# Kernel optimization log

Hardware: AMD Instinct MI355X
Metric: run time of the kernel (lower is better)

Reference implementation:

```python
import jax, jax.numpy as jnp
import numpy as np

N = 100000       # num nodes
E = 3200000      # train message edges (avg degree 32)
EP = 1600000     # pos (and neg) decode edges
F_IN = 128       # node feature dim
H1, H2 = 50, 10  # GCN layer widths from source


def setup_inputs() -> dict:
    key = jax.random.key(0)
    ks = jax.random.split(key, 6)
    x = jax.random.normal(ks[0], (N, F_IN), dtype=jnp.float32)
    train_pos_edge_index = jax.random.randint(ks[1], (2, E), 0, N)
    pos_edge_index = jax.random.randint(ks[2], (2, EP), 0, N)
    neg_edge_index = jax.random.randint(ks[3], (2, EP), 0, N)
    W1 = jax.random.normal(ks[4], (F_IN, H1), dtype=jnp.float32) / np.float32(np.sqrt(F_IN))
    b1 = jnp.zeros((H1,), jnp.float32)
    W2 = jax.random.normal(ks[5], (H1, H2), dtype=jnp.float32) / np.float32(np.sqrt(H1))
    b2 = jnp.zeros((H2,), jnp.float32)
    return {"x": x, "W1": W1, "b1": b1, "W2": W2, "b2": b2,
            "train_pos_edge_index": train_pos_edge_index,
            "pos_edge_index": pos_edge_index,
            "neg_edge_index": neg_edge_index}


def gcn_conv(x, W, b, src, dst, num_nodes):
    # x: [N, Fin] -> transform first (PyG GCNConv), then normalize+aggregate.
    h = x @ W                                                        # [N, Fout]
    deg = jax.ops.segment_sum(jnp.ones(src.shape, h.dtype), dst,
                              num_segments=num_nodes)                # in-degree incl self-loops
    dinv = jnp.where(deg > 0, jax.lax.rsqrt(deg), 0.0)
    norm = dinv[src] * dinv[dst]                                     # [E']
    msgs = h[src] * norm[:, None]                                    # gather + scale
    out = jax.ops.segment_sum(msgs, dst, num_segments=num_nodes)     # scatter-add
    return out + b


def reference(x, W1, b1, W2, b2, train_pos_edge_index, pos_edge_index, neg_edge_index):
    # GCNConv adds self-loops to the message edge set.
    loops = jnp.arange(N, dtype=train_pos_edge_index.dtype)
    src = jnp.concatenate([train_pos_edge_index[0], loops])
    dst = jnp.concatenate([train_pos_edge_index[1], loops])
    # encode(): conv1 -> relu -> conv2
    h = jax.nn.relu(gcn_conv(x, W1, b1, src, dst, N))                # [N, 50]
    z = gcn_conv(h, W2, b2, src, dst, N)                             # [N, 10]
    # decode(): concat pos/neg edges, edge-wise dot product of endpoint embeddings
    ei = jnp.concatenate([pos_edge_index, neg_edge_index], axis=-1)  # [2, 2*EP]
    logits = jnp.sum(z[ei[0]] * z[ei[1]], axis=-1)                   # [2*EP]
    return logits
```

## Files before the change

### kernel.cpp

```cpp
#include <hip/hip_runtime.h>

#define FIN 128
#define H1_ 50
#define H2_ 10
#define ST2S 16

#define BKT_SHIFT 7
#define BKT_W 128
#define NB_MAX 800
#define SB_SHIFT 11
#define SB_W 2048
#define NSB_MAX 64
#define SB_CAP 81920
#define P1_CHUNK 8192
#define P1F_CHUNK 4096


__device__ inline float bf2f(unsigned int u16) {
    union { unsigned int i; float f; } c; c.i = u16 << 16; return c.f;
}
__device__ inline unsigned short f2bf(float f) {
    union { float f; unsigned int i; } c; c.f = f;
    unsigned int x = c.i;
    return (unsigned short)((x + 0x7FFFu + ((x >> 16) & 1u)) >> 16);
}
__device__ inline void unpack8(uint4 v, float* f) {
    f[0] = bf2f(v.x & 0xFFFFu); f[1] = bf2f(v.x >> 16);
    f[2] = bf2f(v.y & 0xFFFFu); f[3] = bf2f(v.y >> 16);
    f[4] = bf2f(v.z & 0xFFFFu); f[5] = bf2f(v.z >> 16);
    f[6] = bf2f(v.w & 0xFFFFu); f[7] = bf2f(v.w >> 16);
}


__global__ __launch_bounds__(256) void partition_sb(const int* __restrict__ src,
                                                    const int* __restrict__ dst,
                                                    int* __restrict__ sbcnt,
                                                    int* __restrict__ bcnt,
                                                    int* __restrict__ pairbuf1,
                                                    int E, int nsb) {
    __shared__ int lh[NB_MAX];
    __shared__ int lhs[NSB_MAX];
    __shared__ int lbs[NSB_MAX];
    int tid = threadIdx.x;
    for (int i = tid; i < NB_MAX; i += 256) lh[i] = 0;
    if (tid < NSB_MAX) lhs[tid] = 0;
    __syncthreads();
    int lo = blockIdx.x * P1_CHUNK;
    int hi = min(lo + P1_CHUNK, E);
    for (int e = lo + tid; e < hi; e += 256)
        atomicAdd(&lh[dst[e] >> BKT_SHIFT], 1);
    __syncthreads();
    if (tid < nsb) {
        int c = 0;
#pragma unroll
        for (int j = 0; j < 16; ++j) {
            int idx = tid * 16 + j;
            c += (idx < NB_MAX) ? lh[idx] : 0;
        }
        lbs[tid] = c ? (tid * SB_CAP + atomicAdd(&sbcnt[tid], c)) : 0;
    }
    for (int i = tid; i < NB_MAX; i += 256) {
        int c = lh[i];
        if (c) atomicAdd(&bcnt[i], c);
    }
    __syncthreads();
    for (int e = lo + tid; e < hi; e += 256) {
        int sv = src[e], d = dst[e];
        int b = d >> SB_SHIFT;
        int r = atomicAdd(&lhs[b], 1);
        pairbuf1[lbs[b] + r] = sv | ((d & (SB_W - 1)) << 17);
    }
}

__global__ __launch_bounds__(256) void bucket_scan(const int* __restrict__ bcnt,
                                                   int* __restrict__ bbase,
                                                   int* __restrict__ bcursor,
                                                   int nb2, int E) {
    __shared__ int s[256];
    int t = threadIdx.x;
    int base = t * 4;
    int v0 = (base + 0 < nb2) ? bcnt[base + 0] : 0;
    int v1 = (base + 1 < nb2) ? bcnt[base + 1] : 0;
    int v2 = (base + 2 < nb2) ? bcnt[base + 2] : 0;
    int v3 = (base + 3 < nb2) ? bcnt[base + 3] : 0;
    int tsum = v0 + v1 + v2 + v3;
    s[t] = tsum;
    __syncthreads();
    for (int off = 1; off < 256; off <<= 1) {
        int x = (t >= off) ? s[t - off] : 0;
        __syncthreads();
        s[t] += x;
        __syncthreads();
    }
    int excl = s[t] - tsum;
    if (t == 0) bbase[nb2] = E;
    if (base + 0 < nb2) { bbase[base + 0] = excl; bcursor[base + 0] = excl; }
    excl += v0;
    if (base + 1 < nb2) { bbase[base + 1] = excl; bcursor[base + 1] = excl; }
    excl += v1;
    if (base + 2 < nb2) { bbase[base + 2] = excl; bcursor[base + 2] = excl; }
    excl += v2;
    if (base + 3 < nb2) { bbase[base + 3] = excl; bcursor[base + 3] = excl; }
}


__global__ __launch_bounds__(256) void partition_fine(const int* __restrict__ pairbuf1,
                                                      const int* __restrict__ sbcnt,
                                                      int* __restrict__ bcursor,
                                                      int* __restrict__ pairbuf2) {
    int sb = blockIdx.y;
    int cnt = sbcnt[sb];
    int rel = blockIdx.x * P1F_CHUNK;
    if (rel >= cnt) return;
    int lo = sb * SB_CAP + rel;
    int hi = sb * SB_CAP + min(rel + P1F_CHUNK, cnt);
    __shared__ int lh[16];
    __shared__ int lb[16];
    int tid = threadIdx.x;
    if (tid < 16) lh[tid] = 0;
    __syncthreads();
    for (int j = lo + tid; j < hi; j += 256)
        atomicAdd(&lh[(pairbuf1[j] >> 17) >> BKT_SHIFT], 1);
    __syncthreads();
    if (tid < 16) {
        int c = lh[tid];
        lb[tid] = c ? atomicAdd(&bcursor[sb * 16 + tid], c) : 0;
        lh[tid] = 0;
    }
    __syncthreads();
    for (int j = lo + tid; j < hi; j += 256) {
        int p = pairbuf1[j];
        int din = p >> 17;
        int fb = din >> BKT_SHIFT;
        int r = atomicAdd(&lh[fb], 1);
        pairbuf2[lb[fb] + r] = (p & 0x1FFFF) | ((din & (BKT_W - 1)) << 17);
    }
}


__global__ __launch_bounds__(256) void bucket_fill_scan(const int* __restrict__ pairbuf,
                                                        const int* __restrict__ bbase,
                                                        int* __restrict__ rowptr,
                                                        float* __restrict__ dinv,
                                                        int* __restrict__ ecol,
                                                        int N, int E) {
    __shared__ int cnt[BKT_W];
    __shared__ int sc[BKT_W];
    __shared__ int cur[BKT_W];
    int b = blockIdx.x;
    int base_node = b << BKT_SHIFT;
    int nnodes = min(BKT_W, N - base_node);
    int tid = threadIdx.x;
    if (tid < BKT_W) cnt[tid] = 0;
    __syncthreads();
    int lo = bbase[b], hi = bbase[b + 1];
    for (int j = lo + tid; j < hi; j += 256)
        atomicAdd(&cnt[pairbuf[j] >> 17], 1);
    __syncthreads();
    int c = (tid < BKT_W) ? cnt[tid] : 0;
    if (tid < BKT_W) sc[tid] = c;
    __syncthreads();
    for (int off = 1; off < BKT_W; off <<= 1) {
        int xv = (tid >= off && tid < BKT_W) ? sc[tid - off] : 0;
        __syncthreads();
        if (tid < BKT_W) sc[tid] += xv;
        __syncthreads();
    }
    if (tid < nnodes) {
        int rp = lo + sc[tid] - c;
        rowptr[base_node + tid] = rp;
        cur[tid] = rp;
        dinv[base_node + tid] = rsqrtf(1.0f + (float)c);
    }
    __syncthreads();
    for (int j = lo + tid; j < hi; j += 256) {
        int p = pairbuf[j];
        int pos = atomicAdd(&cur[p >> 17], 1);
        ecol[pos] = p & 0x1FFFF;
    }
    if (b == (int)gridDim.x - 1 && tid == 0) rowptr[N] = E;
}


#define G1_NODES 128
#define SX_PITCH 132
#define KCHUNK 32
__global__ __launch_bounds__(256) void gemm1_kernel(const float* __restrict__ x,
                                                    const float* __restrict__ W1,
                                                    const float* __restrict__ dinv,
                                                    unsigned short* __restrict__ st1p, int N) {
    __shared__ float sX[G1_NODES * SX_PITCH];
    __shared__ float sW[KCHUNK * 64];
    int tid = threadIdx.x;
    int nb = blockIdx.x * G1_NODES;
    {
        const float4* x4 = (const float4*)(x + (size_t)nb * FIN);
        for (int i = tid; i < G1_NODES * 32; i += 256) {
            int ln = i >> 5, kk = i & 31;
            float4 v = (nb + ln < N) ? x4[(size_t)ln * 32 + kk]
                                     : make_float4(0.f, 0.f, 0.f, 0.f);
            *(float4*)(&sX[ln * SX_PITCH + kk * 4]) = v;
        }
    }
    int q = tid >> 3;
    int g = tid & 7;
    const float* xr0 = &sX[(4 * q + 0) * SX_PITCH];
    const float* xr1 = &sX[(4 * q + 1) * SX_PITCH];
    const float* xr2 = &sX[(4 * q + 2) * SX_PITCH];
    const float* xr3 = &sX[(4 * q + 3) * SX_PITCH];
    float acc[4][8];
#pragma unroll
    for (int i = 0; i < 4; ++i)
#pragma unroll
        for (int j = 0; j < 8; ++j) acc[i][j] = 0.0f;

    for (int kc = 0; kc < FIN / KCHUNK; ++kc) {
        __syncthreads();
        for (int i = tid; i < KCHUNK * 64; i += 256) {
            int k = i >> 6, f = i & 63;
            sW[i] = (f < H1_) ? W1[(kc * KCHUNK + k) * H1_ + f] : 0.0f;
        }
        __syncthreads();
        int kb = kc * KCHUNK;
#pragma unroll 4
        for (int k = 0; k < KCHUNK; ++k) {
            float xv0 = xr0[kb + k];
            float xv1 = xr1[kb + k];
            float xv2 = xr2[kb + k];
            float xv3 = xr3[kb + k];
            const float* w = &sW[k * 64 + g * 8];
#pragma unroll
            for (int j = 0; j < 8; ++j) {
                float wv = w[j];
                acc[0][j] = fmaf(xv0, wv, acc[0][j]);
                acc[1][j] = fmaf(xv1, wv, acc[1][j]);
                acc[2][j] = fmaf(xv2, wv, acc[2][j]);
                acc[3][j] = fmaf(xv3, wv, acc[3][j]);
            }
        }
    }
#pragma unroll
    for (int i = 0; i < 4; ++i) {
        int node = nb + 4 * q + i;
        if (node >= N) continue;
        float di = dinv[node];
        unsigned short o[8];
#pragma unroll
        for (int j = 0; j < 8; ++j) o[j] = f2bf(acc[i][j] * di);
        uint4 pk;
        pk.x = (unsigned)o[0] | ((unsigned)o[1] << 16);
        pk.y = (unsigned)o[2] | ((unsigned)o[3] << 16);
        pk.z = (unsigned)o[4] | ((unsigned)o[5] << 16);
        pk.w = (unsigned)o[6] | ((unsigned)o[7] << 16);
        *(uint4*)(st1p + (size_t)node * 64 + g * 8) = pk;
    }
}


__global__ __launch_bounds__(256) void csr_aggregate1(const unsigned short* __restrict__ st,
                                                      const int* __restrict__ rowptr,
                                                      const int* __restrict__ ecol,
                                                      const float* __restrict__ dinv,
                                                      const float* __restrict__ b,
                                                      float* __restrict__ out, int N) {
    int idx = blockIdx.x * blockDim.x + threadIdx.x;
    if (idx >= N * 8) return;
    int d = idx >> 3;
    int g = idx & 7;
    if (g == 7) return;
    const unsigned short* row = st + g * 8;
    float acc[8];
    {
        uint4 sv = *(const uint4*)(row + (size_t)d * 64);
        float f[8]; unpack8(sv, f);
#pragma unroll
        for (int k = 0; k < 8; ++k) acc[k] = f[k];
    }
    int j = rowptr[d], end = rowptr[d + 1];
    for (; j + 3 < end; j += 4) {
        int s0 = ecol[j], s1 = ecol[j + 1], s2 = ecol[j + 2], s3 = ecol[j + 3];
        uint4 v0 = *(const uint4*)(row + (size_t)s0 * 64);
        uint4 v1 = *(const uint4*)(row + (size_t)s1 * 64);
        uint4 v2 = *(const uint4*)(row + (size_t)s2 * 64);
        uint4 v3 = *(const uint4*)(row + (size_t)s3 * 64);
        float f0[8], f1[8], f2[8], f3[8];
        unpack8(v0, f0); unpack8(v1, f1); unpack8(v2, f2); unpack8(v3, f3);
#pragma unroll
        for (int k = 0; k < 8; ++k) acc[k] += (f0[k] + f1[k]) + (f2[k] + f3[k]);
    }
    for (; j < end; ++j) {
        uint4 v = *(const uint4*)(row + (size_t)ecol[j] * 64);
        float f[8]; unpack8(v, f);
#pragma unroll
        for (int k = 0; k < 8; ++k) acc[k] += f[k];
    }
    float vd = dinv[d];
    int fb = 8 * g;
    float* op = out + (size_t)d * H1_ + fb;
    int npair = (g == 6) ? 1 : 4;
#pragma unroll
    for (int k = 0; k < 4; ++k) {
        if (k >= npair) break;
        float r0 = fmaxf(fmaf(vd, acc[2 * k],     b[fb + 2 * k]),     0.0f);
        float r1 = fmaxf(fmaf(vd, acc[2 * k + 1], b[fb + 2 * k + 1]), 0.0f);
        *(float2*)(op + 2 * k) = make_float2(r0, r1);
    }
}


__global__ __launch_bounds__(256) void gemm2_kernel(const float* __restrict__ h,
                                                    const float* __restrict__ W2,
                                                    const float* __restrict__ dinv,
                                                    float* __restrict__ st2, int n16) {
    __shared__ float sW[H1_ * H2_];
    int tid = threadIdx.x;
    for (int i = tid; i < H1_ * H2_; i += 256) sW[i] = W2[i];
    __syncthreads();
    int idx = blockIdx.x * blockDim.x + tid;
    if (idx >= n16) return;
    int node = idx >> 4;
    int f    = idx & 15;
    if (f >= H2_) { st2[idx] = 0.0f; return; }
    const float* hr = &h[(size_t)node * H1_];
    float acc = 0.0f;
#pragma unroll
    for (int k = 0; k < H1_; ++k) acc = fmaf(hr[k], sW[k * H2_ + f], acc);
    st2[idx] = acc * dinv[node];
}


__global__ __launch_bounds__(256) void csr_aggregate2(const float* __restrict__ st,
                                                      const int* __restrict__ rowptr,
                                                      const int* __restrict__ ecol,
                                                      const float* __restrict__ dinv,
                                                      const float* __restrict__ b,
                                                      float* __restrict__ z0,
                                                      float* __restrict__ z1, int N) {
    int idx = blockIdx.x * blockDim.x + threadIdx.x;
    if (idx >= N * 4) return;
    int d = idx >> 2;
    int g = idx & 3;
    if (g == 3) return;
    const float* row = st + g * 4;
    float4 acc = *(const float4*)(row + (size_t)d * ST2S);
    int j = rowptr[d], end = rowptr[d + 1];
    for (; j + 3 < end; j += 4) {
        int s0 = ecol[j], s1 = ecol[j + 1], s2 = ecol[j + 2], s3 = ecol[j + 3];
        float4 a0 = *(const float4*)(row + (size_t)s0 * ST2S);
        float4 a1 = *(const float4*)(row + (size_t)s1 * ST2S);
        float4 a2 = *(const float4*)(row + (size_t)s2 * ST2S);
        float4 a3 = *(const float4*)(row + (size_t)s3 * ST2S);
        acc.x += (a0.x + a1.x) + (a2.x + a3.x);
        acc.y += (a0.y + a1.y) + (a2.y + a3.y);
        acc.z += (a0.z + a1.z) + (a2.z + a3.z);
        acc.w += (a0.w + a1.w) + (a2.w + a3.w);
    }
    for (; j < end; ++j) {
        float4 a = *(const float4*)(row + (size_t)ecol[j] * ST2S);
        acc.x += a.x; acc.y += a.y; acc.z += a.z; acc.w += a.w;
    }
    float vd = dinv[d];
    if (g < 2) {
        float4 r;
        r.x = fmaf(vd, acc.x, b[4 * g + 0]);
        r.y = fmaf(vd, acc.y, b[4 * g + 1]);
        r.z = fmaf(vd, acc.z, b[4 * g + 2]);
        r.w = fmaf(vd, acc.w, b[4 * g + 3]);
        *(float4*)(z0 + (size_t)d * 8 + 4 * g) = r;
    } else {
        float2 r;
        r.x = fmaf(vd, acc.x, b[8]);
        r.y = fmaf(vd, acc.y, b[9]);
        *(float2*)(z1 + (size_t)d * 2) = r;
    }
}


__global__ __launch_bounds__(256) void decode_kernel(const float* __restrict__ z0,
                                                     const float* __restrict__ z1,
                                                     const int* __restrict__ pos,
                                                     const int* __restrict__ neg,
                                                     float* __restrict__ logits, int EP) {
    int i = blockIdx.x * blockDim.x + threadIdx.x;
    if (i >= 2 * EP) return;
    int a, b;
    if (i < EP) {
        a = __builtin_nontemporal_load(&pos[i]);
        b = __builtin_nontemporal_load(&pos[EP + i]);
    } else {
        int j = i - EP;
        a = __builtin_nontemporal_load(&neg[j]);
        b = __builtin_nontemporal_load(&neg[EP + j]);
    }
    const float4* za = (const float4*)(z0 + (size_t)a * 8);
    const float4* zb = (const float4*)(z0 + (size_t)b * 8);
    float4 a0 = za[0];
    float4 a1 = za[1];
    float4 b0 = zb[0];
    float4 b1 = zb[1];
    float2 a2 = *(const float2*)(z1 + (size_t)a * 2);
    float2 b2 = *(const float2*)(z1 + (size_t)b * 2);
    float acc = a0.x * b0.x;
    acc = fmaf(a0.y, b0.y, acc);
    acc = fmaf(a0.z, b0.z, acc);
    acc = fmaf(a0.w, b0.w, acc);
    acc = fmaf(a1.x, b1.x, acc);
    acc = fmaf(a1.y, b1.y, acc);
    acc = fmaf(a1.z, b1.z, acc);
    acc = fmaf(a1.w, b1.w, acc);
    acc = fmaf(a2.x, b2.x, acc);
    acc = fmaf(a2.y, b2.y, acc);
    __builtin_nontemporal_store(acc, &logits[i]);
}


extern "C" void kernel_launch(void* const* d_in, const int* in_sizes, int n_in,
                              void* d_out, int out_size, void* d_ws, size_t ws_size,
                              hipStream_t stream) {
    const float* x   = (const float*)d_in[0];
    const float* W1  = (const float*)d_in[1];
    const float* b1  = (const float*)d_in[2];
    const float* W2  = (const float*)d_in[3];
    const float* b2  = (const float*)d_in[4];
    const int* train = (const int*)d_in[5];
    const int* pos   = (const int*)d_in[6];
    const int* neg   = (const int*)d_in[7];

    const int N  = in_sizes[0] / FIN;
    const int E  = in_sizes[5] / 2;
    const int EP = in_sizes[6] / 2;

    const int* tsrc = train;
    const int* tdst = train + E;

    size_t off = 0;
    int* rowptr   = (int*)d_ws;              off += (size_t)N + 1;
    int* bcnt     = (int*)d_ws + off;        off += NB_MAX;
    int* sbcnt    = (int*)d_ws + off;        off += NSB_MAX;
    int* bbase    = (int*)d_ws + off;        off += NB_MAX + 1;
    int* bcursor  = (int*)d_ws + off;        off += NB_MAX;
    float* dinv   = (float*)d_ws + off;      off += N;
    off = (off + 15) & ~(size_t)15;
    float* regA   = (float*)d_ws + off;      off += (size_t)32 * N;
    float* regB   = (float*)d_ws + off;
    int* pairbuf2 = (int*)regA;
    unsigned short* st1p = (unsigned short*)regA;
    float* st2    = regA;
    float* z0     = regA + (size_t)16 * N;
    float* z1     = regA + (size_t)24 * N;
    int* pairbuf1 = (int*)regB;
    float* out1   = regB;
    int* ecol     = (int*)d_out;
    float* logits = (float*)d_out;

    const int NB2 = (N + BKT_W - 1) >> BKT_SHIFT;
    const int NSB = (N + SB_W - 1) >> SB_SHIFT;
    const int P1B = (E + P1_CHUNK - 1) / P1_CHUNK;
    const int P1FB = (SB_CAP + P1F_CHUNK - 1) / P1F_CHUNK;

    hipMemsetAsync(bcnt, 0, (NB_MAX + NSB_MAX) * sizeof(int), stream);
    partition_sb<<<P1B, 256, 0, stream>>>(tsrc, tdst, sbcnt, bcnt, pairbuf1, E, NSB);
    bucket_scan<<<1, 256, 0, stream>>>(bcnt, bbase, bcursor, NB2, E);
    partition_fine<<<dim3(P1FB, NSB), 256, 0, stream>>>(pairbuf1, sbcnt, bcursor, pairbuf2);
    bucket_fill_scan<<<NB2, 256, 0, stream>>>(pairbuf2, bbase, rowptr, dinv, ecol, N, E);

    gemm1_kernel<<<(N + G1_NODES - 1) / G1_NODES, 256, 0, stream>>>(x, W1, dinv, st1p, N);
    csr_aggregate1<<<(N * 8 + 255) / 256, 256, 0, stream>>>(
        st1p, rowptr, ecol, dinv, b1, out1, N);

    gemm2_kernel<<<(N * 16 + 255) / 256, 256, 0, stream>>>(out1, W2, dinv, st2, N * 16);
    csr_aggregate2<<<(N * 4 + 255) / 256, 256, 0, stream>>>(
        st2, rowptr, ecol, dinv, b2, z0, z1, N);

    decode_kernel<<<(2 * EP + 255) / 256, 256, 0, stream>>>(z0, z1, pos, neg, logits, EP);
}
```

Measured before the change: 478.3 us.

## Split aggregation tables into feature slices so each gather set fits in cache

The layer-1 bf16 message table is stored as three 16-feature slices of 32 bytes per node plus a 2-feature tail. The layer-1 aggregation runs as four launches, one per slice, and layer-2 is split the same way into an 8-wide and a 2-wide table. Each launch gathers from a much smaller table (about 3.2 MB instead of 12.8 MB), so the random neighbour reads are more likely to hit in L2/MALL. In exchange the CSR index array is re-read once per slice, and edge-index loads and output stores are marked nontemporal.

```diff
diff --git a/kernel.cpp b/kernel.cpp
--- a/kernel.cpp
+++ b/kernel.cpp
@@ -3,7 +3,6 @@
 #define FIN 128
 #define H1_ 50
 #define H2_ 10
-#define ST2S 16
 
 #define BKT_SHIFT 7
 #define BKT_W 128
@@ -15,6 +14,9 @@
 #define P1_CHUNK 8192
 #define P1F_CHUNK 4096
 
+typedef float f32x2 __attribute__((ext_vector_type(2)));
+typedef float f32x4 __attribute__((ext_vector_type(4)));
+
 
 __device__ inline float bf2f(unsigned int u16) {
     union { unsigned int i; float f; } c; c.i = u16 << 16; return c.f;
@@ -29,6 +31,14 @@
     f[2] = bf2f(v.y & 0xFFFFu); f[3] = bf2f(v.y >> 16);
     f[4] = bf2f(v.z & 0xFFFFu); f[5] = bf2f(v.z >> 16);
     f[6] = bf2f(v.w & 0xFFFFu); f[7] = bf2f(v.w >> 16);
+}
+__device__ inline void nt_store2(float* p, float a, float b) {
+    f32x2 v; v.x = a; v.y = b;
+    __builtin_nontemporal_store(v, (f32x2*)p);
+}
+__device__ inline void nt_store4(float* p, float a, float b, float c, float d) {
+    f32x4 v; v.x = a; v.y = b; v.z = c; v.w = d;
+    __builtin_nontemporal_store(v, (f32x4*)p);
 }
 
 
@@ -188,7 +198,7 @@
 __global__ __launch_bounds__(256) void gemm1_kernel(const float* __restrict__ x,
                                                     const float* __restrict__ W1,
                                                     const float* __restrict__ dinv,
-                                                    unsigned short* __restrict__ st1p, int N) {
+                                                    unsigned short* __restrict__ st1, int N) {
     __shared__ float sX[G1_NODES * SX_PITCH];
     __shared__ float sW[KCHUNK * 64];
     int tid = threadIdx.x;
@@ -243,75 +253,119 @@
     for (int i = 0; i < 4; ++i) {
         int node = nb + 4 * q + i;
         if (node >= N) continue;
+        if (g == 7) continue;
         float di = dinv[node];
         unsigned short o[8];
 #pragma unroll
         for (int j = 0; j < 8; ++j) o[j] = f2bf(acc[i][j] * di);
-        uint4 pk;
-        pk.x = (unsigned)o[0] | ((unsigned)o[1] << 16);
-        pk.y = (unsigned)o[2] | ((unsigned)o[3] << 16);
-        pk.z = (unsigned)o[4] | ((unsigned)o[5] << 16);
-        pk.w = (unsigned)o[6] | ((unsigned)o[7] << 16);
-        *(uint4*)(st1p + (size_t)node * 64 + g * 8) = pk;
-    }
-}
-
-
-__global__ __launch_bounds__(256) void csr_aggregate1(const unsigned short* __restrict__ st,
+        if (g < 6) {
+            uint4 pk;
+            pk.x = (unsigned)o[0] | ((unsigned)o[1] << 16);
+            pk.y = (unsigned)o[2] | ((unsigned)o[3] << 16);
+            pk.z = (unsigned)o[4] | ((unsigned)o[5] << 16);
+            pk.w = (unsigned)o[6] | ((unsigned)o[7] << 16);
+            *(uint4*)(st1 + (size_t)(g >> 1) * 16 * N + (size_t)node * 16 + (g & 1) * 8) = pk;
+        } else {
+            unsigned int pk = (unsigned)o[0] | ((unsigned)o[1] << 16);
+            *(unsigned int*)(st1 + (size_t)48 * N + (size_t)node * 2) = pk;
+        }
+    }
+}
+
+
+__global__ __launch_bounds__(256) void csr_agg1_slice(const unsigned short* __restrict__ tab,
                                                       const int* __restrict__ rowptr,
                                                       const int* __restrict__ ecol,
                                                       const float* __restrict__ dinv,
                                                       const float* __restrict__ b,
-                                                      float* __restrict__ out, int N) {
+                                                      float* __restrict__ out,
+                                                      int N) {
     int idx = blockIdx.x * blockDim.x + threadIdx.x;
-    if (idx >= N * 8) return;
-    int d = idx >> 3;
-    int g = idx & 7;
-    if (g == 7) return;
-    const unsigned short* row = st + g * 8;
+    if (idx >= N * 2) return;
+    int d = idx >> 1;
+    int g = idx & 1;
+    const unsigned short* row = tab + g * 8;
     float acc[8];
     {
-        uint4 sv = *(const uint4*)(row + (size_t)d * 64);
+        uint4 sv = *(const uint4*)(row + (size_t)d * 16);
         float f[8]; unpack8(sv, f);
 #pragma unroll
         for (int k = 0; k < 8; ++k) acc[k] = f[k];
     }
     int j = rowptr[d], end = rowptr[d + 1];
     for (; j + 3 < end; j += 4) {
-        int s0 = ecol[j], s1 = ecol[j + 1], s2 = ecol[j + 2], s3 = ecol[j + 3];
-        uint4 v0 = *(const uint4*)(row + (size_t)s0 * 64);
-        uint4 v1 = *(const uint4*)(row + (size_t)s1 * 64);
-        uint4 v2 = *(const uint4*)(row + (size_t)s2 * 64);
-        uint4 v3 = *(const uint4*)(row + (size_t)s3 * 64);
+        int s0 = __builtin_nontemporal_load(&ecol[j]);
+        int s1 = __builtin_nontemporal_load(&ecol[j + 1]);
+        int s2 = __builtin_nontemporal_load(&ecol[j + 2]);
+        int s3 = __builtin_nontemporal_load(&ecol[j + 3]);
+        uint4 v0 = *(const uint4*)(row + (size_t)s0 * 16);
+        uint4 v1 = *(const uint4*)(row + (size_t)s1 * 16);
+        uint4 v2 = *(const uint4*)(row + (size_t)s2 * 16);
+        uint4 v3 = *(const uint4*)(row + (size_t)s3 * 16);
         float f0[8], f1[8], f2[8], f3[8];
         unpack8(v0, f0); unpack8(v1, f1); unpack8(v2, f2); unpack8(v3, f3);
 #pragma unroll
         for (int k = 0; k < 8; ++k) acc[k] += (f0[k] + f1[k]) + (f2[k] + f3[k]);
     }
     for (; j < end; ++j) {
-        uint4 v = *(const uint4*)(row + (size_t)ecol[j] * 64);
+        int s = __builtin_nontemporal_load(&ecol[j]);
+        uint4 v = *(const uint4*)(row + (size_t)s * 16);
         float f[8]; unpack8(v, f);
 #pragma unroll
         for (int k = 0; k < 8; ++k) acc[k] += f[k];
     }
     float vd = dinv[d];
-    int fb = 8 * g;
-    float* op = out + (size_t)d * H1_ + fb;
-    int npair = (g == 6) ? 1 : 4;
+    float* op = out + (size_t)d * H1_ + 8 * g;
 #pragma unroll
     for (int k = 0; k < 4; ++k) {
-        if (k >= npair) break;
-        float r0 = fmaxf(fmaf(vd, acc[2 * k],     b[fb + 2 * k]),     0.0f);
-        float r1 = fmaxf(fmaf(vd, acc[2 * k + 1], b[fb + 2 * k + 1]), 0.0f);
-        *(float2*)(op + 2 * k) = make_float2(r0, r1);
-    }
+        float r0 = fmaxf(fmaf(vd, acc[2 * k],     b[8 * g + 2 * k]),     0.0f);
+        float r1 = fmaxf(fmaf(vd, acc[2 * k + 1], b[8 * g + 2 * k + 1]), 0.0f);
+        nt_store2(op + 2 * k, r0, r1);
+    }
+}
+
+
+__global__ __launch_bounds__(256) void csr_agg1_mini(const unsigned short* __restrict__ tab,
+                                                     const int* __restrict__ rowptr,
+                                                     const int* __restrict__ ecol,
+                                                     const float* __restrict__ dinv,
+                                                     const float* __restrict__ b,
+                                                     float* __restrict__ out, int N) {
+    int d = blockIdx.x * blockDim.x + threadIdx.x;
+    if (d >= N) return;
+    unsigned int sv = *(const unsigned int*)(tab + (size_t)d * 2);
+    float acc0 = bf2f(sv & 0xFFFFu), acc1 = bf2f(sv >> 16);
+    int j = rowptr[d], end = rowptr[d + 1];
+    for (; j + 3 < end; j += 4) {
+        int s0 = __builtin_nontemporal_load(&ecol[j]);
+        int s1 = __builtin_nontemporal_load(&ecol[j + 1]);
+        int s2 = __builtin_nontemporal_load(&ecol[j + 2]);
+        int s3 = __builtin_nontemporal_load(&ecol[j + 3]);
+        unsigned int v0 = *(const unsigned int*)(tab + (size_t)s0 * 2);
+        unsigned int v1 = *(const unsigned int*)(tab + (size_t)s1 * 2);
+        unsigned int v2 = *(const unsigned int*)(tab + (size_t)s2 * 2);
+        unsigned int v3 = *(const unsigned int*)(tab + (size_t)s3 * 2);
+        acc0 += (bf2f(v0 & 0xFFFFu) + bf2f(v1 & 0xFFFFu)) + (bf2f(v2 & 0xFFFFu) + bf2f(v3 & 0xFFFFu));
+        acc1 += (bf2f(v0 >> 16) + bf2f(v1 >> 16)) + (bf2f(v2 >> 16) + bf2f(v3 >> 16));
+    }
+    for (; j < end; ++j) {
+        int s = __builtin_nontemporal_load(&ecol[j]);
+        unsigned int v = *(const unsigned int*)(tab + (size_t)s * 2);
+        acc0 += bf2f(v & 0xFFFFu);
+        acc1 += bf2f(v >> 16);
+    }
+    float vd = dinv[d];
+    float r0 = fmaxf(fmaf(vd, acc0, b[48]), 0.0f);
+    float r1 = fmaxf(fmaf(vd, acc1, b[49]), 0.0f);
+    nt_store2(out + (size_t)d * H1_ + 48, r0, r1);
 }
 
 
 __global__ __launch_bounds__(256) void gemm2_kernel(const float* __restrict__ h,
                                                     const float* __restrict__ W2,
                                                     const float* __restrict__ dinv,
-                                                    float* __restrict__ st2, int n16) {
+                                                    float* __restrict__ st2a,
+                                                    float* __restrict__ st2b, int n16) {
     __shared__ float sW[H1_ * H2_];
     int tid = threadIdx.x;
     for (int i = tid; i < H1_ * H2_; i += 256) sW[i] = W2[i];
@@ -320,59 +374,87 @@
     if (idx >= n16) return;
     int node = idx >> 4;
     int f    = idx & 15;
-    if (f >= H2_) { st2[idx] = 0.0f; return; }
+    if (f >= H2_) return;
     const float* hr = &h[(size_t)node * H1_];
     float acc = 0.0f;
 #pragma unroll
     for (int k = 0; k < H1_; ++k) acc = fmaf(hr[k], sW[k * H2_ + f], acc);
-    st2[idx] = acc * dinv[node];
-}
-
-
-__global__ __launch_bounds__(256) void csr_aggregate2(const float* __restrict__ st,
-                                                      const int* __restrict__ rowptr,
-                                                      const int* __restrict__ ecol,
-                                                      const float* __restrict__ dinv,
-                                                      const float* __restrict__ b,
-                                                      float* __restrict__ z0,
-                                                      float* __restrict__ z1, int N) {
+    float v = acc * dinv[node];
+    if (f < 8) st2a[(size_t)node * 8 + f] = v;
+    else       st2b[(size_t)node * 2 + (f - 8)] = v;
+}
+
+
+__global__ __launch_bounds__(256) void csr_agg2_a(const float* __restrict__ st,
+                                                  const int* __restrict__ rowptr,
+                                                  const int* __restrict__ ecol,
+                                                  const float* __restrict__ dinv,
+                                                  const float* __restrict__ b,
+                                                  float* __restrict__ z0, int N) {
     int idx = blockIdx.x * blockDim.x + threadIdx.x;
-    if (idx >= N * 4) return;
-    int d = idx >> 2;
-    int g = idx & 3;
-    if (g == 3) return;
+    if (idx >= N * 2) return;
+    int d = idx >> 1;
+    int g = idx & 1;
     const float* row = st + g * 4;
-    float4 acc = *(const float4*)(row + (size_t)d * ST2S);
+    float4 acc = *(const float4*)(row + (size_t)d * 8);
     int j = rowptr[d], end = rowptr[d + 1];
     for (; j + 3 < end; j += 4) {
-        int s0 = ecol[j], s1 = ecol[j + 1], s2 = ecol[j + 2], s3 = ecol[j + 3];
-        float4 a0 = *(const float4*)(row + (size_t)s0 * ST2S);
-        float4 a1 = *(const float4*)(row + (size_t)s1 * ST2S);
-        float4 a2 = *(const float4*)(row + (size_t)s2 * ST2S);
-        float4 a3 = *(const float4*)(row + (size_t)s3 * ST2S);
+        int s0 = __builtin_nontemporal_load(&ecol[j]);
+        int s1 = __builtin_nontemporal_load(&ecol[j + 1]);
+        int s2 = __builtin_nontemporal_load(&ecol[j + 2]);
+        int s3 = __builtin_nontemporal_load(&ecol[j + 3]);
+        float4 a0 = *(const float4*)(row + (size_t)s0 * 8);
+        float4 a1 = *(const float4*)(row + (size_t)s1 * 8);
+        float4 a2 = *(const float4*)(row + (size_t)s2 * 8);
+        float4 a3 = *(const float4*)(row + (size_t)s3 * 8);
         acc.x += (a0.x + a1.x) + (a2.x + a3.x);
         acc.y += (a0.y + a1.y) + (a2.y + a3.y);
         acc.z += (a0.z + a1.z) + (a2.z + a3.z);
         acc.w += (a0.w + a1.w) + (a2.w + a3.w);
     }
     for (; j < end; ++j) {
-        float4 a = *(const float4*)(row + (size_t)ecol[j] * ST2S);
+        int s = __builtin_nontemporal_load(&ecol[j]);
+        float4 a = *(const float4*)(row + (size_t)s * 8);
         acc.x += a.x; acc.y += a.y; acc.z += a.z; acc.w += a.w;
     }
     float vd = dinv[d];
-    if (g < 2) {
-        float4 r;
-        r.x = fmaf(vd, acc.x, b[4 * g + 0]);
-        r.y = fmaf(vd, acc.y, b[4 * g + 1]);
-        r.z = fmaf(vd, acc.z, b[4 * g + 2]);
-        r.w = fmaf(vd, acc.w, b[4 * g + 3]);
-        *(float4*)(z0 + (size_t)d * 8 + 4 * g) = r;
-    } else {
-        float2 r;
-        r.x = fmaf(vd, acc.x, b[8]);
-        r.y = fmaf(vd, acc.y, b[9]);
-        *(float2*)(z1 + (size_t)d * 2) = r;
-    }
+    nt_store4(z0 + (size_t)d * 8 + 4 * g,
+              fmaf(vd, acc.x, b[4 * g + 0]),
+              fmaf(vd, acc.y, b[4 * g + 1]),
+              fmaf(vd, acc.z, b[4 * g + 2]),
+              fmaf(vd, acc.w, b[4 * g + 3]));
+}
+
+
+__global__ __launch_bounds__(256) void csr_agg2_b(const float* __restrict__ st,
+                                                  const int* __restrict__ rowptr,
+                                                  const int* __restrict__ ecol,
+                                                  const float* __restrict__ dinv,
+                                                  const float* __restrict__ b,
+                                                  float* __restrict__ z1, int N) {
+    int d = blockIdx.x * blockDim.x + threadIdx.x;
+    if (d >= N) return;
+    float2 acc = *(const float2*)(st + (size_t)d * 2);
+    int j = rowptr[d], end = rowptr[d + 1];
+    for (; j + 3 < end; j += 4) {
+        int s0 = __builtin_nontemporal_load(&ecol[j]);
+        int s1 = __builtin_nontemporal_load(&ecol[j + 1]);
+        int s2 = __builtin_nontemporal_load(&ecol[j + 2]);
+        int s3 = __builtin_nontemporal_load(&ecol[j + 3]);
+        float2 a0 = *(const float2*)(st + (size_t)s0 * 2);
+        float2 a1 = *(const float2*)(st + (size_t)s1 * 2);
+        float2 a2 = *(const float2*)(st + (size_t)s2 * 2);
+        float2 a3 = *(const float2*)(st + (size_t)s3 * 2);
+        acc.x += (a0.x + a1.x) + (a2.x + a3.x);
+        acc.y += (a0.y + a1.y) + (a2.y + a3.y);
+    }
+    for (; j < end; ++j) {
+        int s = __builtin_nontemporal_load(&ecol[j]);
+        float2 a = *(const float2*)(st + (size_t)s * 2);
+        acc.x += a.x; acc.y += a.y;
+    }
+    float vd = dinv[d];
+    nt_store2(z1 + (size_t)d * 2, fmaf(vd, acc.x, b[8]), fmaf(vd, acc.y, b[9]));
 }
 
 
@@ -444,10 +526,11 @@
     float* regA   = (float*)d_ws + off;      off += (size_t)32 * N;
     float* regB   = (float*)d_ws + off;
     int* pairbuf2 = (int*)regA;
-    unsigned short* st1p = (unsigned short*)regA;
-    float* st2    = regA;
-    float* z0     = regA + (size_t)16 * N;
-    float* z1     = regA + (size_t)24 * N;
+    unsigned short* st1 = (unsigned short*)regA;
+    float* st2a   = regA;
+    float* st2b   = regA + (size_t)8 * N;
+    float* z0     = regA + (size_t)10 * N;
+    float* z1     = regA + (size_t)18 * N;
     int* pairbuf1 = (int*)regB;
     float* out1   = regB;
     int* ecol     = (int*)d_out;
@@ -464,13 +547,16 @@
     partition_fine<<<dim3(P1FB, NSB), 256, 0, stream>>>(pairbuf1, sbcnt, bcursor, pairbuf2);
     bucket_fill_scan<<<NB2, 256, 0, stream>>>(pairbuf2, bbase, rowptr, dinv, ecol, N, E);
 
-    gemm1_kernel<<<(N + G1_NODES - 1) / G1_NODES, 256, 0, stream>>>(x, W1, dinv, st1p, N);
-    csr_aggregate1<<<(N * 8 + 255) / 256, 256, 0, stream>>>(
-        st1p, rowptr, ecol, dinv, b1, out1, N);
-
-    gemm2_kernel<<<(N * 16 + 255) / 256, 256, 0, stream>>>(out1, W2, dinv, st2, N * 16);
-    csr_aggregate2<<<(N * 4 + 255) / 256, 256, 0, stream>>>(
-        st2, rowptr, ecol, dinv, b2, z0, z1, N);
+    gemm1_kernel<<<(N + G1_NODES - 1) / G1_NODES, 256, 0, stream>>>(x, W1, dinv, st1, N);
+    for (int s = 0; s < 3; ++s)
+        csr_agg1_slice<<<(N * 2 + 255) / 256, 256, 0, stream>>>(
+            st1 + (size_t)s * 16 * N, rowptr, ecol, dinv, b1 + 16 * s, out1 + 16 * s, N);
+    csr_agg1_mini<<<(N + 255) / 256, 256, 0, stream>>>(
+        st1 + (size_t)48 * N, rowptr, ecol, dinv, b1, out1, N);
+
+    gemm2_kernel<<<(N * 16 + 255) / 256, 256, 0, stream>>>(out1, W2, dinv, st2a, st2b, N * 16);
+    csr_agg2_a<<<(N * 2 + 255) / 256, 256, 0, stream>>>(st2a, rowptr, ecol, dinv, b2, z0, N);
+    csr_agg2_b<<<(N + 255) / 256, 256, 0, stream>>>(st2b, rowptr, ecol, dinv, b2, z1, N);
 
     decode_kernel<<<(2 * EP + 255) / 256, 256, 0, stream>>>(z0, z1, pos, neg, logits, EP);
 }
```

New measurement: 615.8 us. +28.7%, slower.

## Sort CSR columns by source chunk and narrow aggregate1 to 2 features per thread

Applied to the files above, without the earlier changes.

The bucket fill now counts each destination's edges in 16 sub-bins keyed by source-index range. It prefix-sums those bins so ecol comes out roughly sorted by source within each row, which should improve gather locality in later aggregations. csr_aggregate1 changes from 8 bf16 features per thread with 16-byte loads to 2 features per thread with 4-byte loads, across 25 threads per node. This gives more parallelism and adjacent threads read contiguous bytes of the same source row, at the cost of more threads re-reading the edge list. gemm1 also skips storing the unused padding group.

```diff
diff --git a/kernel.cpp b/kernel.cpp
--- a/kernel.cpp
+++ b/kernel.cpp
@@ -14,6 +14,7 @@
 #define SB_CAP 81920
 #define P1_CHUNK 8192
 #define P1F_CHUNK 4096
+#define SCH 16
 
 
 __device__ inline float bf2f(unsigned int u16) {
@@ -23,12 +24,6 @@
     union { float f; unsigned int i; } c; c.f = f;
     unsigned int x = c.i;
     return (unsigned short)((x + 0x7FFFu + ((x >> 16) & 1u)) >> 16);
-}
-__device__ inline void unpack8(uint4 v, float* f) {
-    f[0] = bf2f(v.x & 0xFFFFu); f[1] = bf2f(v.x >> 16);
-    f[2] = bf2f(v.y & 0xFFFFu); f[3] = bf2f(v.y >> 16);
-    f[4] = bf2f(v.z & 0xFFFFu); f[5] = bf2f(v.z >> 16);
-    f[6] = bf2f(v.w & 0xFFFFu); f[7] = bf2f(v.w >> 16);
 }
 
 
@@ -144,21 +139,26 @@
                                                         float* __restrict__ dinv,
                                                         int* __restrict__ ecol,
                                                         int N, int E) {
-    __shared__ int cnt[BKT_W];
+    __shared__ int cnt2[BKT_W * SCH];
     __shared__ int sc[BKT_W];
-    __shared__ int cur[BKT_W];
     int b = blockIdx.x;
     int base_node = b << BKT_SHIFT;
     int nnodes = min(BKT_W, N - base_node);
     int tid = threadIdx.x;
-    if (tid < BKT_W) cnt[tid] = 0;
+    for (int i = tid; i < BKT_W * SCH; i += 256) cnt2[i] = 0;
     __syncthreads();
     int lo = bbase[b], hi = bbase[b + 1];
-    for (int j = lo + tid; j < hi; j += 256)
-        atomicAdd(&cnt[pairbuf[j] >> 17], 1);
-    __syncthreads();
-    int c = (tid < BKT_W) ? cnt[tid] : 0;
-    if (tid < BKT_W) sc[tid] = c;
+    for (int j = lo + tid; j < hi; j += 256) {
+        int p = pairbuf[j];
+        atomicAdd(&cnt2[(p >> 17) * SCH + ((p & 0x1FFFF) >> 13)], 1);
+    }
+    __syncthreads();
+    int tsum = 0;
+    if (tid < BKT_W) {
+#pragma unroll
+        for (int c = 0; c < SCH; ++c) tsum += cnt2[tid * SCH + c];
+        sc[tid] = tsum;
+    }
     __syncthreads();
     for (int off = 1; off < BKT_W; off <<= 1) {
         int xv = (tid >= off && tid < BKT_W) ? sc[tid - off] : 0;
@@ -167,16 +167,23 @@
         __syncthreads();
     }
     if (tid < nnodes) {
-        int rp = lo + sc[tid] - c;
+        int rp = lo + sc[tid] - tsum;
         rowptr[base_node + tid] = rp;
-        cur[tid] = rp;
-        dinv[base_node + tid] = rsqrtf(1.0f + (float)c);
+        dinv[base_node + tid] = rsqrtf(1.0f + (float)tsum);
+        int run = rp;
+#pragma unroll
+        for (int c = 0; c < SCH; ++c) {
+            int v = cnt2[tid * SCH + c];
+            cnt2[tid * SCH + c] = run;
+            run += v;
+        }
     }
     __syncthreads();
     for (int j = lo + tid; j < hi; j += 256) {
         int p = pairbuf[j];
-        int pos = atomicAdd(&cur[p >> 17], 1);
-        ecol[pos] = p & 0x1FFFF;
+        int s = p & 0x1FFFF;
+        int pos = atomicAdd(&cnt2[(p >> 17) * SCH + (s >> 13)], 1);
+        ecol[pos] = s;
     }
     if (b == (int)gridDim.x - 1 && tid == 0) rowptr[N] = E;
 }
@@ -243,6 +250,7 @@
     for (int i = 0; i < 4; ++i) {
         int node = nb + 4 * q + i;
         if (node >= N) continue;
+        if (g == 7) continue;
         float di = dinv[node];
         unsigned short o[8];
 #pragma unroll
@@ -257,6 +265,7 @@
 }
 
 
+#define F2 25
 __global__ __launch_bounds__(256) void csr_aggregate1(const unsigned short* __restrict__ st,
                                                       const int* __restrict__ rowptr,
                                                       const int* __restrict__ ecol,
@@ -264,47 +273,32 @@
                                                       const float* __restrict__ b,
                                                       float* __restrict__ out, int N) {
     int idx = blockIdx.x * blockDim.x + threadIdx.x;
-    if (idx >= N * 8) return;
-    int d = idx >> 3;
-    int g = idx & 7;
-    if (g == 7) return;
-    const unsigned short* row = st + g * 8;
-    float acc[8];
-    {
-        uint4 sv = *(const uint4*)(row + (size_t)d * 64);
-        float f[8]; unpack8(sv, f);
-#pragma unroll
-        for (int k = 0; k < 8; ++k) acc[k] = f[k];
-    }
+    if (idx >= N * F2) return;
+    int d  = idx / F2;
+    int fp = idx - d * F2;
+    int fo = 2 * fp;
+    unsigned int self2 = *(const unsigned int*)(st + (size_t)d * 64 + fo);
+    float acc0 = bf2f(self2 & 0xFFFFu);
+    float acc1 = bf2f(self2 >> 16);
     int j = rowptr[d], end = rowptr[d + 1];
     for (; j + 3 < end; j += 4) {
         int s0 = ecol[j], s1 = ecol[j + 1], s2 = ecol[j + 2], s3 = ecol[j + 3];
-        uint4 v0 = *(const uint4*)(row + (size_t)s0 * 64);
-        uint4 v1 = *(const uint4*)(row + (size_t)s1 * 64);
-        uint4 v2 = *(const uint4*)(row + (size_t)s2 * 64);
-        uint4 v3 = *(const uint4*)(row + (size_t)s3 * 64);
-        float f0[8], f1[8], f2[8], f3[8];
-        unpack8(v0, f0); unpack8(v1, f1); unpack8(v2, f2); unpack8(v3, f3);
-#pragma unroll
-        for (int k = 0; k < 8; ++k) acc[k] += (f0[k] + f1[k]) + (f2[k] + f3[k]);
+        unsigned int v0 = *(const unsigned int*)(st + (size_t)s0 * 64 + fo);
+        unsigned int v1 = *(const unsigned int*)(st + (size_t)s1 * 64 + fo);
+        unsigned int v2 = *(const unsigned int*)(st + (size_t)s2 * 64 + fo);
+        unsigned int v3 = *(const unsigned int*)(st + (size_t)s3 * 64 + fo);
+        acc0 += (bf2f(v0 & 0xFFFFu) + bf2f(v1 & 0xFFFFu)) + (bf2f(v2 & 0xFFFFu) + bf2f(v3 & 0xFFFFu));
+        acc1 += (bf2f(v0 >> 16) + bf2f(v1 >> 16)) + (bf2f(v2 >> 16) + bf2f(v3 >> 16));
     }
     for (; j < end; ++j) {
-        uint4 v = *(const uint4*)(row + (size_t)ecol[j] * 64);
-        float f[8]; unpack8(v, f);
-#pragma unroll
-        for (int k = 0; k < 8; ++k) acc[k] += f[k];
+        unsigned int v = *(const unsigned int*)(st + (size_t)ecol[j] * 64 + fo);
+        acc0 += bf2f(v & 0xFFFFu);
+        acc1 += bf2f(v >> 16);
     }
     float vd = dinv[d];
-    int fb = 8 * g;
-    float* op = out + (size_t)d * H1_ + fb;
-    int npair = (g == 6) ? 1 : 4;
-#pragma unroll
-    for (int k = 0; k < 4; ++k) {
-        if (k >= npair) break;
-        float r0 = fmaxf(fmaf(vd, acc[2 * k],     b[fb + 2 * k]),     0.0f);
-        float r1 = fmaxf(fmaf(vd, acc[2 * k + 1], b[fb + 2 * k + 1]), 0.0f);
-        *(float2*)(op + 2 * k) = make_float2(r0, r1);
-    }
+    float r0 = fmaxf(fmaf(vd, acc0, b[fo]),     0.0f);
+    float r1 = fmaxf(fmaf(vd, acc1, b[fo + 1]), 0.0f);
+    *(float2*)(out + (size_t)d * H1_ + fo) = make_float2(r0, r1);
 }
 
 
@@ -465,7 +459,7 @@
     bucket_fill_scan<<<NB2, 256, 0, stream>>>(pairbuf2, bbase, rowptr, dinv, ecol, N, E);
 
     gemm1_kernel<<<(N + G1_NODES - 1) / G1_NODES, 256, 0, stream>>>(x, W1, dinv, st1p, N);
-    csr_aggregate1<<<(N * 8 + 255) / 256, 256, 0, stream>>>(
+    csr_aggregate1<<<(N * F2 + 255) / 256, 256, 0, stream>>>(
         st1p, rowptr, ecol, dinv, b1, out1, N);
 
     gemm2_kernel<<<(N * 16 + 255) / 256, 256, 0, stream>>>(out1, W2, dinv, st2, N * 16);
```

Result: faster. 457.8 us (-4.3%).
